# Optimization experiments

Measured on AMD Instinct MI355X. Metric: run time of the kernel, lower is better.

The kernel has to match this reference:

```python
import jax, jax.numpy as jnp
import numpy as np

L, B, S, D, H = 2, 4, 2048, 512, 8
HD = D // H
FF = 4 * D
EPS = 1e-5


def _ln(x, g, b):
    m = jnp.mean(x, axis=-1, keepdims=True)
    v = jnp.mean((x - m) ** 2, axis=-1, keepdims=True)
    return (x - m) * jax.lax.rsqrt(v + EPS) * g + b


def setup_inputs() -> dict:
    key = jax.random.key(0)
    ks = jax.random.split(key, 8)
    w_scale = 0.02
    return {
        "q": jax.random.normal(ks[0], (B, S, D), jnp.float32),
        "ln1_g": jnp.ones((L, D), jnp.float32),
        "ln1_b": jnp.zeros((L, D), jnp.float32),
        "wq": jax.random.normal(ks[1], (L, D, D), jnp.float32) * w_scale,
        "bq": jnp.zeros((L, D), jnp.float32),
        "wk": jax.random.normal(ks[2], (L, D, D), jnp.float32) * w_scale,
        "bk": jnp.zeros((L, D), jnp.float32),
        "wv": jax.random.normal(ks[3], (L, D, D), jnp.float32) * w_scale,
        "bv": jnp.zeros((L, D), jnp.float32),
        "wo": jax.random.normal(ks[4], (L, D, D), jnp.float32) * w_scale,
        "bo": jnp.zeros((L, D), jnp.float32),
        "ln2_g": jnp.ones((L, D), jnp.float32),
        "ln2_b": jnp.zeros((L, D), jnp.float32),
        "w1": jax.random.normal(ks[5], (L, D, FF), jnp.float32) * w_scale,
        "b1": jnp.zeros((L, FF), jnp.float32),
        "w2": jax.random.normal(ks[6], (L, FF, D), jnp.float32) * w_scale,
        "b2": jnp.zeros((L, D), jnp.float32),
    }


def reference(q, ln1_g, ln1_b, wq, bq, wk, bk, wv, bv, wo, bo,
              ln2_g, ln2_b, w1, b1, w2, b2):
    # Faithful to TransformerEncoder: k, v are fixed to the ORIGINAL q input
    # for every layer (only q updates through the stack).
    b, s, d = q.shape
    scaling = float(HD) ** -0.5
    k_in = q
    v_in = q
    x = q
    for l in range(L):
        residual = x
        qn = _ln(x, ln1_g[l], ln1_b[l])
        kn = _ln(k_in, ln1_g[l], ln1_b[l])
        vn = _ln(v_in, ln1_g[l], ln1_b[l])
        qh = (qn @ wq[l] + bq[l]).reshape(b, s, H, HD).transpose(0, 2, 1, 3)
        kh = (kn @ wk[l] + bk[l]).reshape(b, s, H, HD).transpose(0, 2, 1, 3)
        vh = (vn @ wv[l] + bv[l]).reshape(b, s, H, HD).transpose(0, 2, 1, 3)
        # [B,H,Sq,Sk] full score tensor, as in the original module
        scores = jnp.einsum("bhqe,bhke->bhqk", qh, kh) * scaling
        attn = jax.nn.softmax(scores, axis=-1)
        out = jnp.einsum("bhqk,bhke->bhqe", attn, vh)
        out = out.transpose(0, 2, 1, 3).reshape(b, s, d)
        out = out @ wo[l] + bo[l]
        x = residual + out
        residual = x
        y = _ln(x, ln2_g[l], ln2_b[l])
        y = jax.nn.relu(y @ w1[l] + b1[l]) @ w2[l] + b2[l]
        x = residual + y
    return x
```

## Files before the change

### kernel.cpp

```cpp
#include <hip/hip_runtime.h>

typedef unsigned short u16;
typedef __bf16 bf16x8 __attribute__((ext_vector_type(8)));
typedef float f32x4 __attribute__((ext_vector_type(4)));

#define DEV static __device__ __forceinline__

DEV u16 f2bf(float f) {
    union { float f; unsigned u; } a; a.f = f;
    unsigned r = a.u + 0x7fffu + ((a.u >> 16) & 1u);
    return (u16)(r >> 16);
}

DEV f32x4 fzero() { f32x4 z; z[0]=0.f; z[1]=0.f; z[2]=0.f; z[3]=0.f; return z; }

DEV bf16x8 load8(const u16* p) {
    uint4 u = *(const uint4*)p;
    union { uint4 u; bf16x8 b; } c; c.u = u; return c.b;
}

DEV f32x4 mfma16(bf16x8 a, bf16x8 b, f32x4 c) {
    return __builtin_amdgcn_mfma_f32_16x16x32_bf16(a, b, c, 0, 0, 0);
}

typedef __attribute__((address_space(1))) void as1_void;
typedef __attribute__((address_space(3))) void as3_void;

DEV void async16(const u16* g, u16* lds) {
    __builtin_amdgcn_global_load_lds((as1_void*)g, (as3_void*)lds, 16, 0, 0);
}

__global__ __launch_bounds__(256)
void prep(const float* __restrict__ wq, const float* __restrict__ wk,
          const float* __restrict__ wv, const float* __restrict__ wo,
          const float* __restrict__ w1, const float* __restrict__ w2,
          const float* __restrict__ bq, const float* __restrict__ bk,
          const float* __restrict__ bv, u16* __restrict__ wT,
          float* __restrict__ bqkv) {
    const int bid = blockIdx.x;
    if (bid >= 6144) {
        int i = bid - 6144;
        int l = i / 6, idx = (i % 6) * 256 + threadIdx.x;
        float v = idx < 512 ? bq[l * 512 + idx]
                : idx < 1024 ? bk[l * 512 + idx - 512]
                : bv[l * 512 + idx - 1024];
        bqkv[l * 1536 + idx] = v;
        return;
    }
    const int l = bid / 3072, t = bid % 3072;
    u16* base = wT + (size_t)l * 3145728;
    const size_t o512 = (size_t)l * 262144, o1m = (size_t)l * 1048576;
    const float* src; u16* dst; int K, N, tn, tk;
    if (t < 1024) {
        int m = t >> 8, r = t & 255;
        src = m == 0 ? wq + o512 : m == 1 ? wk + o512 : m == 2 ? wv + o512 : wo + o512;
        dst = base + (size_t)m * 262144;
        K = 512; N = 512; tn = r & 15; tk = r >> 4;
    } else if (t < 2048) {
        int r = t - 1024;
        src = w1 + o1m; dst = base + 1048576;
        K = 512; N = 2048; tn = r & 63; tk = r >> 6;
    } else {
        int r = t - 2048;
        src = w2 + o1m; dst = base + 2097152;
        K = 2048; N = 512; tn = r & 15; tk = r >> 4;
    }
    __shared__ float tile[32][33];
    const int tx = threadIdx.x & 31, ty = threadIdx.x >> 5;
    const int n0 = tn * 32, k0 = tk * 32;
#pragma unroll
    for (int i = 0; i < 4; i++)
        tile[ty + i * 8][tx] = src[(size_t)(k0 + ty + i * 8) * N + n0 + tx];
    __syncthreads();
#pragma unroll
    for (int i = 0; i < 4; i++)
        dst[(size_t)(n0 + ty + i * 8) * K + k0 + tx] = f2bf(tile[tx][ty + i * 8]);
}

DEV void ln_body(const float* xr, const float* g, const float* bb, u16* orow) {
    const int t = threadIdx.x;
    float v0 = xr[t], v1 = xr[t + 256];
    float s = v0 + v1, s2 = v0 * v0 + v1 * v1;
#pragma unroll
    for (int off = 32; off > 0; off >>= 1) {
        s  += __shfl_down(s,  off);
        s2 += __shfl_down(s2, off);
    }
    __shared__ float red[8];
    const int w = t >> 6, ln = t & 63;
    if (ln == 0) { red[w] = s; red[4 + w] = s2; }
    __syncthreads();
    s  = red[0] + red[1] + red[2] + red[3];
    s2 = red[4] + red[5] + red[6] + red[7];
    float mean = s * (1.f / 512.f);
    float var  = s2 * (1.f / 512.f) - mean * mean;
    float rstd = rsqrtf(var + 1e-5f);
    orow[t]       = f2bf((v0 - mean) * rstd * g[t]       + bb[t]);
    orow[t + 256] = f2bf((v1 - mean) * rstd * g[t + 256] + bb[t + 256]);
}

__global__ __launch_bounds__(256)
void ln_k(const float* __restrict__ x, const float* __restrict__ g,
          const float* __restrict__ bb, u16* __restrict__ o) {
    const int row = blockIdx.x;
    ln_body(x + (size_t)row * 512, g, bb, o + (size_t)row * 512);
}

__global__ __launch_bounds__(256)
void lnd_k(const float* __restrict__ x0, u16* __restrict__ o0,
           const float* __restrict__ x1, u16* __restrict__ o1,
           const float* __restrict__ g, const float* __restrict__ bb) {
    const int row = blockIdx.x;
    const float* x = blockIdx.y ? x1 : x0;
    u16* o = blockIdx.y ? o1 : o0;
    ln_body(x + (size_t)row * 512, g, bb, o + (size_t)row * 512);
}

template<int BN, int EPI>
__global__ __launch_bounds__(256, 2)
void gemm_k(const u16* __restrict__ A, const u16* __restrict__ Bt,
            const float* __restrict__ bias, const float* __restrict__ res,
            void* __restrict__ outp, int M, int N, int K) {
    __shared__ u16 As[2][128 * 32];
    __shared__ u16 Bs[2][BN * 32];
    const int tid = threadIdx.x, w = tid >> 6, ln = tid & 63;
    const int m0 = blockIdx.x * 128, n0 = blockIdx.y * BN;
    const int wr = (w >> 1) * 64, wc = (w & 1) * (BN / 2);
    const int l15 = ln & 15, l4 = ln >> 4;
    constexpr int NI = BN / 32;

    f32x4 acc[4][NI];
#pragma unroll
    for (int mi = 0; mi < 4; mi++)
#pragma unroll
        for (int ni = 0; ni < NI; ni++) acc[mi][ni] = fzero();

    auto stage = [&](int buf, int k0) {
#pragma unroll
        for (int i = 0; i < 2; i++) {
            int chunk = i * 4 + w;
            int r = chunk * 16 + (ln >> 2);
            const u16* gp = A + (size_t)(m0 + r) * K + k0 + (ln & 3) * 8;
            async16(gp, &As[buf][chunk * 512]);
        }
#pragma unroll
        for (int i = 0; i < BN / 64; i++) {
            int chunk = i * 4 + w;
            int r = chunk * 16 + (ln >> 2);
            const u16* gp = Bt + (size_t)(n0 + r) * K + k0 + (ln & 3) * 8;
            async16(gp, &Bs[buf][chunk * 512]);
        }
    };

    stage(0, 0);
    __syncthreads();
    const int nk = K / 32;
    for (int kt = 0; kt < nk; ++kt) {
        const int cur = kt & 1;
        if (kt + 1 < nk) stage(cur ^ 1, (kt + 1) * 32);
        bf16x8 a[4], b[NI];
#pragma unroll
        for (int mi = 0; mi < 4; mi++)
            a[mi] = load8(&As[cur][(wr + mi * 16 + l15) * 32 + l4 * 8]);
#pragma unroll
        for (int ni = 0; ni < NI; ni++)
            b[ni] = load8(&Bs[cur][(wc + ni * 16 + l15) * 32 + l4 * 8]);
#pragma unroll
        for (int mi = 0; mi < 4; mi++)
#pragma unroll
            for (int ni = 0; ni < NI; ni++)
                acc[mi][ni] = mfma16(a[mi], b[ni], acc[mi][ni]);
        __syncthreads();
    }

#pragma unroll
    for (int mi = 0; mi < 4; mi++)
#pragma unroll
        for (int ni = 0; ni < NI; ni++) {
            int row0 = m0 + wr + mi * 16 + l4 * 4;
            int col  = n0 + wc + ni * 16 + l15;
            float bv = bias[col];
#pragma unroll
            for (int j = 0; j < 4; j++) {
                float v = acc[mi][ni][j] + bv;
                size_t off = (size_t)(row0 + j) * N + col;
                if constexpr (EPI == 2) ((float*)outp)[off] = v + res[off];
                else if constexpr (EPI == 1) ((u16*)outp)[off] = f2bf(v > 0.f ? v : 0.f);
                else ((u16*)outp)[off] = f2bf(v);
            }
        }
}

__global__ __launch_bounds__(256, 2)
void gemm_qkv(const u16* __restrict__ A1, const u16* __restrict__ A2,
              const u16* __restrict__ Bt, const float* __restrict__ bias,
              u16* __restrict__ qkB, u16* __restrict__ vTp) {
    constexpr int K = 512;
    __shared__ u16 As[2][128 * 32];
    __shared__ u16 Bs[2][128 * 32];
    const int tid = threadIdx.x, w = tid >> 6, ln = tid & 63;
    const int m0 = blockIdx.x * 128, n0 = blockIdx.y * 128;
    const int wr = (w >> 1) * 64, wc = (w & 1) * 64;
    const int l15 = ln & 15, l4 = ln >> 4;
    const u16* A = (n0 >= 512) ? A2 : A1;

    f32x4 acc[4][4];
#pragma unroll
    for (int mi = 0; mi < 4; mi++)
#pragma unroll
        for (int ni = 0; ni < 4; ni++) acc[mi][ni] = fzero();

    auto stage = [&](int buf, int k0) {
#pragma unroll
        for (int i = 0; i < 2; i++) {
            int chunk = i * 4 + w;
            int r = chunk * 16 + (ln >> 2);
            async16(A + (size_t)(m0 + r) * K + k0 + (ln & 3) * 8, &As[buf][chunk * 512]);
            async16(Bt + (size_t)(n0 + r) * K + k0 + (ln & 3) * 8, &Bs[buf][chunk * 512]);
        }
    };

    stage(0, 0);
    __syncthreads();
    for (int kt = 0; kt < 16; ++kt) {
        const int cur = kt & 1;
        if (kt + 1 < 16) stage(cur ^ 1, (kt + 1) * 32);
        bf16x8 a[4], b[4];
#pragma unroll
        for (int mi = 0; mi < 4; mi++)
            a[mi] = load8(&As[cur][(wr + mi * 16 + l15) * 32 + l4 * 8]);
#pragma unroll
        for (int ni = 0; ni < 4; ni++)
            b[ni] = load8(&Bs[cur][(wc + ni * 16 + l15) * 32 + l4 * 8]);
#pragma unroll
        for (int mi = 0; mi < 4; mi++)
#pragma unroll
            for (int ni = 0; ni < 4; ni++)
                acc[mi][ni] = mfma16(a[mi], b[ni], acc[mi][ni]);
        __syncthreads();
    }

    if (n0 < 1024) {
        const float scale = (n0 < 512) ? 0.125f : 1.f;
#pragma unroll
        for (int mi = 0; mi < 4; mi++)
#pragma unroll
            for (int ni = 0; ni < 4; ni++) {
                int row0 = m0 + wr + mi * 16 + l4 * 4;
                int col  = n0 + wc + ni * 16 + l15;
                float bv = bias[col];
#pragma unroll
                for (int j = 0; j < 4; j++)
                    qkB[(size_t)(row0 + j) * 1024 + col] = f2bf((acc[mi][ni][j] + bv) * scale);
            }
    } else {
#pragma unroll
        for (int mi = 0; mi < 4; mi++)
#pragma unroll
            for (int ni = 0; ni < 4; ni++) {
                int row0 = m0 + wr + mi * 16 + l4 * 4;
                int col  = n0 + wc + ni * 16 + l15;
                float bv = bias[col];
                int c = col - 1024;
                int bh = (row0 >> 11) * 8 + (c >> 6);
                ushort4 pk;
                pk.x = f2bf(acc[mi][ni][0] + bv);
                pk.y = f2bf(acc[mi][ni][1] + bv);
                pk.z = f2bf(acc[mi][ni][2] + bv);
                pk.w = f2bf(acc[mi][ni][3] + bv);
                *(ushort4*)(vTp + (size_t)bh * 131072 + (size_t)(c & 63) * 2048 + (row0 & 2047)) = pk;
            }
    }
}

__global__ __launch_bounds__(256, 2)
void attn_k(const u16* __restrict__ qh, int qstr, const u16* __restrict__ kh, int kstr,
            const u16* __restrict__ vT, u16* __restrict__ o) {
    __shared__ u16 Kt[2][4096];
    __shared__ u16 Vt[2][4096];
    __shared__ u16 Pl[4][2048];
    const int tid = threadIdx.x, w = tid >> 6, ln = tid & 63;
    const int orig = blockIdx.y * 16 + blockIdx.x;
    const int swz = (orig & 7) * 64 + (orig >> 3);
    const int bx = swz & 15, by = swz >> 4;
    const int b = by >> 3, h = by & 7;
    const int q0 = bx * 128;
    const size_t bS = (size_t)b * 2048;
    const int h64 = h * 64;
    const int l15 = ln & 15, l4 = ln >> 4;

    const int srow = ln >> 3;
    const int scol = ((ln & 7) ^ srow) * 8;

    const u16* qp = qh + (bS + q0 + w * 32 + l15) * qstr + h64;
    bf16x8 qa[2][2];
    qa[0][0] = load8(qp + l4 * 8);
    qa[0][1] = load8(qp + 32 + l4 * 8);
    qa[1][0] = load8(qp + 16 * qstr + l4 * 8);
    qa[1][1] = load8(qp + 16 * qstr + 32 + l4 * 8);

    const u16* kbase = kh + bS * kstr + h64;
    const u16* vbase = vT + (size_t)(b * 8 + h) * 131072;

    auto stage = [&](int buf, int sk) {
#pragma unroll
        for (int i = 0; i < 2; i++) {
            int chunk = i * 4 + w;
            int row = chunk * 8 + srow;
            async16(kbase + (size_t)(sk + row) * kstr + scol, &Kt[buf][chunk * 512]);
            async16(vbase + (size_t)row * 2048 + sk + scol, &Vt[buf][chunk * 512]);
        }
    };

    float l_acc[2];
    f32x4 oacc[2][4];
#pragma unroll
    for (int mf = 0; mf < 2; mf++) {
        l_acc[mf] = 0.f;
#pragma unroll
        for (int j = 0; j < 4; j++) oacc[mf][j] = fzero();
    }

    const int swl = (l15 & 7) << 4;

    stage(0, 0);
    for (int t = 0; t < 32; ++t) {
        const int cur = t & 1;
        __syncthreads();
        if (t < 31) stage(cur ^ 1, (t + 1) * 64);

        const char* KtC = (const char*)Kt[cur];
        const char* VtC = (const char*)Vt[cur];

        f32x4 s[2][4];
#pragma unroll
        for (int ni = 0; ni < 4; ni++) {
            const char* kr = KtC + (ni * 16 + l15) * 128;
            bf16x8 kb0 = load8((const u16*)(kr + ((l4 * 16) ^ swl)));
            bf16x8 kb1 = load8((const u16*)(kr + ((64 + l4 * 16) ^ swl)));
            s[0][ni] = mfma16(kb0, qa[0][0], fzero());
            s[0][ni] = mfma16(kb1, qa[0][1], s[0][ni]);
            s[1][ni] = mfma16(kb0, qa[1][0], fzero());
            s[1][ni] = mfma16(kb1, qa[1][1], s[1][ni]);
        }

        char* Pw = (char*)Pl[w];
#pragma unroll
        for (int mf = 0; mf < 2; mf++) {
            const int qrow = mf * 16 + l15;
            char* Pr = Pw + qrow * 128;
            const int qsw = (qrow & 7) << 4;
#pragma unroll
            for (int ni = 0; ni < 4; ni++) {
                const int boff = ni * 32 + l4 * 8;
#pragma unroll
                for (int jj = 0; jj < 2; jj++) {
                    float p0 = __expf(s[mf][ni][jj * 2]);
                    float p1 = __expf(s[mf][ni][jj * 2 + 1]);
                    union { float f; unsigned u; } c0, c1;
                    c0.f = p0; c1.f = p1;
                    unsigned hi = c1.u & 0xffff0000u;
                    union { unsigned u; float f; } t0, t1;
                    t0.u = c0.u & 0xffff0000u; t1.u = hi;
                    l_acc[mf] += t0.f + t1.f;
                    *(unsigned*)(Pr + ((boff + jj * 4) ^ qsw)) = (c0.u >> 16) | hi;
                }
            }
        }

        bf16x8 pa[2][2];
#pragma unroll
        for (int mf = 0; mf < 2; mf++) {
            pa[mf][0] = load8((const u16*)(Pw + (mf * 16 + l15) * 128 + ((l4 * 16) ^ swl)));
            pa[mf][1] = load8((const u16*)(Pw + (mf * 16 + l15) * 128 + ((64 + l4 * 16) ^ swl)));
        }
#pragma unroll
        for (int hd4 = 0; hd4 < 4; hd4++) {
            const char* vr = VtC + (hd4 * 16 + l15) * 128;
            bf16x8 vb0 = load8((const u16*)(vr + ((l4 * 16) ^ swl)));
            bf16x8 vb1 = load8((const u16*)(vr + ((64 + l4 * 16) ^ swl)));
            oacc[0][hd4] = mfma16(pa[0][0], vb0, oacc[0][hd4]);
            oacc[0][hd4] = mfma16(pa[0][1], vb1, oacc[0][hd4]);
            oacc[1][hd4] = mfma16(pa[1][0], vb0, oacc[1][hd4]);
            oacc[1][hd4] = mfma16(pa[1][1], vb1, oacc[1][hd4]);
        }
    }

    float rlj[2][4];
#pragma unroll
    for (int mf = 0; mf < 2; mf++) {
        l_acc[mf] += __shfl_xor(l_acc[mf], 16);
        l_acc[mf] += __shfl_xor(l_acc[mf], 32);
        float inv = 1.f / l_acc[mf];
#pragma unroll
        for (int j = 0; j < 4; j++)
            rlj[mf][j] = __shfl(inv, (ln & 48) | (l4 * 4 + j));
    }

#pragma unroll
    for (int mf = 0; mf < 2; mf++)
#pragma unroll
        for (int hd4 = 0; hd4 < 4; hd4++)
#pragma unroll
            for (int j = 0; j < 4; j++) {
                float v = oacc[mf][hd4][j] * rlj[mf][j];
                size_t row = bS + q0 + w * 32 + mf * 16 + l4 * 4 + j;
                o[row * 512 + h64 + hd4 * 16 + l15] = f2bf(v);
            }
}

extern "C" void kernel_launch(void* const* d_in, const int* in_sizes, int n_in,
                              void* d_out, int out_size, void* d_ws, size_t ws_size,
                              hipStream_t stream) {
    const float* q    = (const float*)d_in[0];
    const float* ln1g = (const float*)d_in[1];
    const float* ln1b = (const float*)d_in[2];
    const float* wq   = (const float*)d_in[3];
    const float* bq   = (const float*)d_in[4];
    const float* wk   = (const float*)d_in[5];
    const float* bk   = (const float*)d_in[6];
    const float* wv   = (const float*)d_in[7];
    const float* bv   = (const float*)d_in[8];
    const float* wo   = (const float*)d_in[9];
    const float* bo   = (const float*)d_in[10];
    const float* ln2g = (const float*)d_in[11];
    const float* ln2b = (const float*)d_in[12];
    const float* w1   = (const float*)d_in[13];
    const float* b1   = (const float*)d_in[14];
    const float* w2   = (const float*)d_in[15];
    const float* b2   = (const float*)d_in[16];

    char* ws = (char*)d_ws;
    size_t off = 0;
    auto take = [&](size_t bytes) -> char* {
        char* p = ws + off; off += (bytes + 255) & ~(size_t)255; return p;
    };
    u16*   wT   = (u16*)take(6291456ull * 2);
    float* bqkv = (float*)take(2 * 1536 * 4);
    float* xA   = (float*)take(4194304ull * 4);
    float* xB   = (float*)take(4194304ull * 4);
    u16*   qn   = (u16*)take(4194304ull * 2);
    u16*   kn   = (u16*)take(4194304ull * 2);
    u16*   qkB  = (u16*)take(8388608ull * 2);
    u16*   hbuf = (u16*)take(16777216ull * 2);
    u16*   vTb  = hbuf;
    (void)ws_size; (void)in_sizes; (void)n_in; (void)out_size;

    prep<<<6156, 256, 0, stream>>>(wq, wk, wv, wo, w1, w2, bq, bk, bv, wT, bqkv);

    const float* xcur = q;
    for (int l = 0; l < 2; l++) {
        u16* base = wT + (size_t)l * 3145728;
        if (l == 0) {
            ln_k<<<8192, 256, 0, stream>>>(q, ln1g, ln1b, qn);
        } else {
            lnd_k<<<dim3(8192, 2), 256, 0, stream>>>(xcur, qn, q, kn,
                                                     ln1g + 512, ln1b + 512);
        }
        const u16* A2 = (l == 0) ? qn : kn;
        gemm_qkv<<<dim3(64, 12), 256, 0, stream>>>(qn, A2, base, bqkv + l * 1536, qkB, vTb);
        attn_k<<<dim3(16, 32), 256, 0, stream>>>(qkB, 1024, qkB + 512, 1024, vTb, qn);
        gemm_k<64, 2><<<dim3(64, 8), 256, 0, stream>>>(qn, base + 786432, bo + l * 512, xcur, xA, 8192, 512, 512);
        ln_k<<<8192, 256, 0, stream>>>(xA, ln2g + l * 512, ln2b + l * 512, kn);
        gemm_k<128, 1><<<dim3(64, 16), 256, 0, stream>>>(kn, base + 1048576, b1 + l * 2048, nullptr, hbuf, 8192, 2048, 512);
        float* xout = (l == 1) ? (float*)d_out : xB;
        gemm_k<64, 2><<<dim3(64, 8), 256, 0, stream>>>(hbuf, base + 2097152, b2 + l * 512, xA, xout, 8192, 512, 2048);
        xcur = xout;
    }
}
```

Before: 348.6 us.

## Add BK=64 swizzled K-tile path to gemm_k and raise occupancy hints

Adds a BK template parameter to the generic GEMM. The N=512 GEMMs (output projection and FF2) now stage 64-wide K tiles into LDS using an XOR swizzle, which halves the number of K iterations and barriers per tile. Launch bounds for the GEMM, QKV and attention kernels go from 2 to 3 blocks per SM, and the exp/pack loop order in attention is swapped. Capping registers for 3 blocks may cause spills, and the larger LDS tiles may limit how many blocks actually fit.

```diff
diff --git a/kernel.cpp b/kernel.cpp
--- a/kernel.cpp
+++ b/kernel.cpp
@@ -116,13 +116,13 @@
     ln_body(x + (size_t)row * 512, g, bb, o + (size_t)row * 512);
 }
 
-template<int BN, int EPI>
-__global__ __launch_bounds__(256, 2)
+template<int BN, int BK, int EPI>
+__global__ __launch_bounds__(256, 3)
 void gemm_k(const u16* __restrict__ A, const u16* __restrict__ Bt,
             const float* __restrict__ bias, const float* __restrict__ res,
             void* __restrict__ outp, int M, int N, int K) {
-    __shared__ u16 As[2][128 * 32];
-    __shared__ u16 Bs[2][BN * 32];
+    __shared__ u16 As[2][128 * BK];
+    __shared__ u16 Bs[2][BN * BK];
     const int tid = threadIdx.x, w = tid >> 6, ln = tid & 63;
     const int m0 = blockIdx.x * 128, n0 = blockIdx.y * BN;
     const int wr = (w >> 1) * 64, wc = (w & 1) * (BN / 2);
@@ -136,40 +136,78 @@
         for (int ni = 0; ni < NI; ni++) acc[mi][ni] = fzero();
 
     auto stage = [&](int buf, int k0) {
-#pragma unroll
-        for (int i = 0; i < 2; i++) {
-            int chunk = i * 4 + w;
-            int r = chunk * 16 + (ln >> 2);
-            const u16* gp = A + (size_t)(m0 + r) * K + k0 + (ln & 3) * 8;
-            async16(gp, &As[buf][chunk * 512]);
-        }
-#pragma unroll
-        for (int i = 0; i < BN / 64; i++) {
-            int chunk = i * 4 + w;
-            int r = chunk * 16 + (ln >> 2);
-            const u16* gp = Bt + (size_t)(n0 + r) * K + k0 + (ln & 3) * 8;
-            async16(gp, &Bs[buf][chunk * 512]);
+        if constexpr (BK == 32) {
+#pragma unroll
+            for (int i = 0; i < 2; i++) {
+                int chunk = i * 4 + w;
+                int r = chunk * 16 + (ln >> 2);
+                async16(A + (size_t)(m0 + r) * K + k0 + (ln & 3) * 8, &As[buf][chunk * 512]);
+            }
+#pragma unroll
+            for (int i = 0; i < BN / 64; i++) {
+                int chunk = i * 4 + w;
+                int r = chunk * 16 + (ln >> 2);
+                async16(Bt + (size_t)(n0 + r) * K + k0 + (ln & 3) * 8, &Bs[buf][chunk * 512]);
+            }
+        } else {
+            const int srow = ln >> 3;
+            const int scol = ((ln & 7) ^ srow) * 8;
+#pragma unroll
+            for (int i = 0; i < 4; i++) {
+                int chunk = i * 4 + w;
+                int r = chunk * 8 + srow;
+                async16(A + (size_t)(m0 + r) * K + k0 + scol, &As[buf][chunk * 512]);
+            }
+#pragma unroll
+            for (int i = 0; i < BN / 32; i++) {
+                int chunk = i * 4 + w;
+                int r = chunk * 8 + srow;
+                async16(Bt + (size_t)(n0 + r) * K + k0 + scol, &Bs[buf][chunk * 512]);
+            }
         }
     };
 
     stage(0, 0);
     __syncthreads();
-    const int nk = K / 32;
+    const int nk = K / BK;
     for (int kt = 0; kt < nk; ++kt) {
         const int cur = kt & 1;
-        if (kt + 1 < nk) stage(cur ^ 1, (kt + 1) * 32);
-        bf16x8 a[4], b[NI];
-#pragma unroll
-        for (int mi = 0; mi < 4; mi++)
-            a[mi] = load8(&As[cur][(wr + mi * 16 + l15) * 32 + l4 * 8]);
-#pragma unroll
-        for (int ni = 0; ni < NI; ni++)
-            b[ni] = load8(&Bs[cur][(wc + ni * 16 + l15) * 32 + l4 * 8]);
-#pragma unroll
-        for (int mi = 0; mi < 4; mi++)
+        if (kt + 1 < nk) stage(cur ^ 1, (kt + 1) * BK);
+        if constexpr (BK == 32) {
+            bf16x8 a[4], b[NI];
+#pragma unroll
+            for (int mi = 0; mi < 4; mi++)
+                a[mi] = load8(&As[cur][(wr + mi * 16 + l15) * 32 + l4 * 8]);
 #pragma unroll
             for (int ni = 0; ni < NI; ni++)
-                acc[mi][ni] = mfma16(a[mi], b[ni], acc[mi][ni]);
+                b[ni] = load8(&Bs[cur][(wc + ni * 16 + l15) * 32 + l4 * 8]);
+#pragma unroll
+            for (int mi = 0; mi < 4; mi++)
+#pragma unroll
+                for (int ni = 0; ni < NI; ni++)
+                    acc[mi][ni] = mfma16(a[mi], b[ni], acc[mi][ni]);
+        } else {
+            const int swl = (l15 & 7) << 4;
+#pragma unroll
+            for (int ks = 0; ks < 2; ks++) {
+                bf16x8 a[4], b[NI];
+#pragma unroll
+                for (int mi = 0; mi < 4; mi++) {
+                    const char* ba = (const char*)&As[cur][(wr + mi * 16 + l15) * 64];
+                    a[mi] = load8((const u16*)(ba + ((ks * 64 + l4 * 16) ^ swl)));
+                }
+#pragma unroll
+                for (int ni = 0; ni < NI; ni++) {
+                    const char* bb2 = (const char*)&Bs[cur][(wc + ni * 16 + l15) * 64];
+                    b[ni] = load8((const u16*)(bb2 + ((ks * 64 + l4 * 16) ^ swl)));
+                }
+#pragma unroll
+                for (int mi = 0; mi < 4; mi++)
+#pragma unroll
+                    for (int ni = 0; ni < NI; ni++)
+                        acc[mi][ni] = mfma16(a[mi], b[ni], acc[mi][ni]);
+            }
+        }
         __syncthreads();
     }
 
@@ -191,7 +229,7 @@
         }
 }
 
-__global__ __launch_bounds__(256, 2)
+__global__ __launch_bounds__(256, 3)
 void gemm_qkv(const u16* __restrict__ A1, const u16* __restrict__ A2,
               const u16* __restrict__ Bt, const float* __restrict__ bias,
               u16* __restrict__ qkB, u16* __restrict__ vTp) {
@@ -273,7 +311,7 @@
     }
 }
 
-__global__ __launch_bounds__(256, 2)
+__global__ __launch_bounds__(256, 3)
 void attn_k(const u16* __restrict__ qh, int qstr, const u16* __restrict__ kh, int kstr,
             const u16* __restrict__ vT, u16* __restrict__ o) {
     __shared__ u16 Kt[2][4096];
@@ -351,10 +389,10 @@
             char* Pr = Pw + qrow * 128;
             const int qsw = (qrow & 7) << 4;
 #pragma unroll
-            for (int ni = 0; ni < 4; ni++) {
-                const int boff = ni * 32 + l4 * 8;
-#pragma unroll
-                for (int jj = 0; jj < 2; jj++) {
+            for (int jj = 0; jj < 2; jj++)
+#pragma unroll
+                for (int ni = 0; ni < 4; ni++) {
+                    const int boff = ni * 32 + l4 * 8;
                     float p0 = __expf(s[mf][ni][jj * 2]);
                     float p1 = __expf(s[mf][ni][jj * 2 + 1]);
                     union { float f; unsigned u; } c0, c1;
@@ -365,7 +403,6 @@
                     l_acc[mf] += t0.f + t1.f;
                     *(unsigned*)(Pr + ((boff + jj * 4) ^ qsw)) = (c0.u >> 16) | hi;
                 }
-            }
         }
 
         bf16x8 pa[2][2];
@@ -460,11 +497,11 @@
         const u16* A2 = (l == 0) ? qn : kn;
         gemm_qkv<<<dim3(64, 12), 256, 0, stream>>>(qn, A2, base, bqkv + l * 1536, qkB, vTb);
         attn_k<<<dim3(16, 32), 256, 0, stream>>>(qkB, 1024, qkB + 512, 1024, vTb, qn);
-        gemm_k<64, 2><<<dim3(64, 8), 256, 0, stream>>>(qn, base + 786432, bo + l * 512, xcur, xA, 8192, 512, 512);
+        gemm_k<64, 64, 2><<<dim3(64, 8), 256, 0, stream>>>(qn, base + 786432, bo + l * 512, xcur, xA, 8192, 512, 512);
         ln_k<<<8192, 256, 0, stream>>>(xA, ln2g + l * 512, ln2b + l * 512, kn);
-        gemm_k<128, 1><<<dim3(64, 16), 256, 0, stream>>>(kn, base + 1048576, b1 + l * 2048, nullptr, hbuf, 8192, 2048, 512);
+        gemm_k<128, 32, 1><<<dim3(64, 16), 256, 0, stream>>>(kn, base + 1048576, b1 + l * 2048, nullptr, hbuf, 8192, 2048, 512);
         float* xout = (l == 1) ? (float*)d_out : xB;
-        gemm_k<64, 2><<<dim3(64, 8), 256, 0, stream>>>(hbuf, base + 2097152, b2 + l * 512, xA, xout, 8192, 512, 2048);
+        gemm_k<64, 64, 2><<<dim3(64, 8), 256, 0, stream>>>(hbuf, base + 2097152, b2 + l * 512, xA, xout, 8192, 512, 2048);
         xcur = xout;
     }
 }
```

After: 332.9 us. 1.05x faster.
